# Performance work log

Hardware: AMD Instinct MI355X
Metric: run time of the kernel (lower is better)

## Reference

```python
import jax, jax.numpy as jnp
import numpy as np

PIXEL_SIZE = 0.1
PI = 3.141592653589793


def setup_inputs() -> dict:
    key = jax.random.key(0)
    batch = jax.random.normal(key, (128, 1, 512, 512), dtype=jnp.float32)
    return {"batch": batch}


def _hann_window(roi):
    # lin = linspace(-roi/2, roi/2, roi); r[i,j] = sqrt(lin[j]^2 + lin[i]^2)
    lin = jnp.linspace(-roi / 2, roi / 2, roi, dtype=jnp.float32)
    r = jnp.sqrt(lin[None, :] ** 2 + lin[:, None] ** 2)
    hann = 0.5 * (1.0 + jnp.cos(PI * r / (roi / 2)))
    hann = jnp.where(r > roi / 2, 0.0, hann)
    return hann  # [roi, roi]


def _radial_segments(roi, n_freq):
    # radialDst = round(sqrt(xx^2 + yy^2)) with x = arange(-cx, roi-cx)
    cx = roi // 2
    x = np.arange(-cx, roi - cx, dtype=np.float64)
    xx, yy = np.meshgrid(x, x, indexing="ij")
    rad = np.round(np.sqrt(xx ** 2 + yy ** 2)).astype(np.int32)
    # bins >= n_freq go into an overflow segment that is discarded
    seg = np.where(rad < n_freq, rad, n_freq)
    return jnp.asarray(seg.ravel())


def reference(batch):
    px = PIXEL_SIZE
    roi = batch.shape[-1]
    cx = roi // 2
    n_freq = cx + 1
    nyquist = 1.0 / (2.0 * px)

    # subtract per-ROI mean
    batch_nm = batch - jnp.mean(batch, axis=(2, 3), keepdims=True)

    # Hann-windowed 2D power spectrum, averaged over realizations
    hann = _hann_window(roi)[None, None, :, :]
    F = jnp.fft.fftshift(jnp.fft.fft2(batch_nm * hann, axes=(2, 3)), axes=(2, 3))
    ps = jnp.mean(jnp.abs(F) ** 2, axis=0)            # [1, roi, roi]
    nps2D = (px ** 2 / roi ** 2) * jnp.squeeze(ps)    # [roi, roi]

    # single-pass radial mean binning (replaces per-k boolean-mask loop)
    seg = _radial_segments(roi, n_freq)
    flat = nps2D.ravel()
    sums = jax.ops.segment_sum(flat, seg, num_segments=n_freq + 1)[:n_freq]
    counts = jax.ops.segment_sum(jnp.ones_like(flat), seg, num_segments=n_freq + 1)[:n_freq]
    nps1D = sums / counts

    f1D = jnp.linspace(0.0, nyquist, n_freq, dtype=jnp.float32)
    return nps1D, nps2D, f1D
```

## Files before the change

kernel.cpp:

```cpp
#include <hip/hip_runtime.h>
#include <hip/hip_fp16.h>

#define N 512
#define NF 257
#define NB 128
#define PI_F 3.14159265358979323846f
#define C_SQ2 0.70710678118654752440f

__device__ __forceinline__ float2 cmul(float2 a, float2 b) {
    return make_float2(a.x * b.x - a.y * b.y, a.x * b.y + a.y * b.x);
}
__device__ __forceinline__ void bf(float2& a, float2& b) {
    float2 t = b;
    b = make_float2(a.x - t.x, a.y - t.y);
    a = make_float2(a.x + t.x, a.y + t.y);
}
__device__ __forceinline__ void bf_tw(float2& a, float2& b, float2 w) {
    float2 t = cmul(b, w);
    b = make_float2(a.x - t.x, a.y - t.y);
    a = make_float2(a.x + t.x, a.y + t.y);
}
__device__ __forceinline__ void bf_ni(float2& a, float2& b) {
    float2 t = make_float2(b.y, -b.x);
    b = make_float2(a.x - t.x, a.y - t.y);
    a = make_float2(a.x + t.x, a.y + t.y);
}
__device__ __forceinline__ void lds_order() {
    asm volatile("" ::: "memory");
}

__device__ __forceinline__ void fft_phaseA(float2 v[8]) {
    const float2 w64  = make_float2(C_SQ2, -C_SQ2);
    const float2 w192 = make_float2(-C_SQ2, -C_SQ2);
    bf(v[0], v[1]); bf(v[2], v[3]); bf(v[4], v[5]); bf(v[6], v[7]);
    bf(v[0], v[2]); bf_ni(v[1], v[3]); bf(v[4], v[6]); bf_ni(v[5], v[7]);
    bf(v[0], v[4]); bf_tw(v[1], v[5], w64); bf_ni(v[2], v[6]); bf_tw(v[3], v[7], w192);
}
__device__ __forceinline__ void fft_phaseBC(float2 v[8], float2 W1, float2 W1a,
                                            float2 W1n, float2 W1c, float2 W2,
                                            float2 W2n, float2 W3) {
    bf_tw(v[0], v[1], W3); bf_tw(v[2], v[3], W3); bf_tw(v[4], v[5], W3); bf_tw(v[6], v[7], W3);
    bf_tw(v[0], v[2], W2); bf_tw(v[1], v[3], W2n); bf_tw(v[4], v[6], W2); bf_tw(v[5], v[7], W2n);
    bf_tw(v[0], v[4], W1); bf_tw(v[1], v[5], W1a); bf_tw(v[2], v[6], W1n); bf_tw(v[3], v[7], W1c);
}

__device__ __forceinline__ void fft512_core(float2 v[8], float2* st, int l) {
    const float2 w64  = make_float2(C_SQ2, -C_SQ2);
    const float2 w192 = make_float2(-C_SQ2, -C_SQ2);
    int g = l >> 3, r = l & 7;
    lds_order();
    fft_phaseA(v);
#pragma unroll
    for (int e = 0; e < 8; e++) st[9 * l + e] = v[e];
    lds_order();
#pragma unroll
    for (int t = 0; t < 8; t++) v[t] = st[72 * g + 9 * t + r];
    float sn, cs;
    __sincosf(-(PI_F / 32.0f) * (float)r, &sn, &cs);
    float2 W1 = make_float2(cs, sn);
    float2 W2 = cmul(W1, W1);
    float2 W3 = cmul(W2, W2);
    float2 W2n = make_float2(W2.y, -W2.x);
    float2 W1a = cmul(W1, w64);
    float2 W1n = make_float2(W1.y, -W1.x);
    float2 W1c = cmul(W1, w192);
    fft_phaseBC(v, W1, W1a, W1n, W1c, W2, W2n, W3);
    lds_order();
#pragma unroll
    for (int t = 0; t < 8; t++) st[72 * g + 9 * t + r] = v[t];
    lds_order();
#pragma unroll
    for (int t = 0; t < 8; t++) v[t] = st[72 * t + l + (l >> 3)];
    __sincosf(-(PI_F / 256.0f) * (float)l, &sn, &cs);
    float2 Wc = make_float2(cs, sn);
    float2 w2 = cmul(Wc, Wc);
    float2 w4 = cmul(w2, w2);
    float2 w2n = make_float2(w2.y, -w2.x);
    float2 Wca = cmul(Wc, w64);
    float2 Wcn = make_float2(Wc.y, -Wc.x);
    float2 Wcc = cmul(Wc, w192);
    fft_phaseBC(v, Wc, Wca, Wcn, Wcc, w2, w2n, w4);
}

__device__ __forceinline__ void fft512_x2(float2 va[8], float2 vb[8], float2* st, int l) {
    const float2 w64  = make_float2(C_SQ2, -C_SQ2);
    const float2 w192 = make_float2(-C_SQ2, -C_SQ2);
    int g = l >> 3, r = l & 7;
    fft_phaseA(va); fft_phaseA(vb);
    lds_order();
#pragma unroll
    for (int e = 0; e < 8; e++) st[9 * l + e] = va[e];
    lds_order();
#pragma unroll
    for (int t = 0; t < 8; t++) va[t] = st[72 * g + 9 * t + r];
    lds_order();
#pragma unroll
    for (int e = 0; e < 8; e++) st[9 * l + e] = vb[e];
    lds_order();
#pragma unroll
    for (int t = 0; t < 8; t++) vb[t] = st[72 * g + 9 * t + r];
    float sn, cs;
    __sincosf(-(PI_F / 32.0f) * (float)r, &sn, &cs);
    float2 W1 = make_float2(cs, sn);
    float2 W2 = cmul(W1, W1);
    float2 W3 = cmul(W2, W2);
    float2 W2n = make_float2(W2.y, -W2.x);
    float2 W1a = cmul(W1, w64);
    float2 W1n = make_float2(W1.y, -W1.x);
    float2 W1c = cmul(W1, w192);
    fft_phaseBC(va, W1, W1a, W1n, W1c, W2, W2n, W3);
    fft_phaseBC(vb, W1, W1a, W1n, W1c, W2, W2n, W3);
    lds_order();
#pragma unroll
    for (int t = 0; t < 8; t++) st[72 * g + 9 * t + r] = va[t];
    lds_order();
#pragma unroll
    for (int t = 0; t < 8; t++) va[t] = st[72 * t + l + (l >> 3)];
    lds_order();
#pragma unroll
    for (int t = 0; t < 8; t++) st[72 * g + 9 * t + r] = vb[t];
    lds_order();
#pragma unroll
    for (int t = 0; t < 8; t++) vb[t] = st[72 * t + l + (l >> 3)];
    __sincosf(-(PI_F / 256.0f) * (float)l, &sn, &cs);
    float2 Wc = make_float2(cs, sn);
    float2 w2 = cmul(Wc, Wc);
    float2 w4 = cmul(w2, w2);
    float2 w2n = make_float2(w2.y, -w2.x);
    float2 Wca = cmul(Wc, w64);
    float2 Wcn = make_float2(Wc.y, -Wc.x);
    float2 Wcc = cmul(Wc, w192);
    fft_phaseBC(va, Wc, Wca, Wcn, Wcc, w2, w2n, w4);
    fft_phaseBC(vb, Wc, Wca, Wcn, Wcc, w2, w2n, w4);
}

__device__ __forceinline__ void unpack_rows(const float2 v[8], __half2* tile,
                                            int lr0, int lr1, int l, int sl) {
#pragma unroll
    for (int t = 0; t <= 4; t++) {
        float2 a = v[7 - t];
        float zfx = __shfl(a.x, sl);
        float zfy = __shfl(a.y, sl);
        if (l == 0) { float2 o = v[(8 - t) & 7]; zfx = o.x; zfy = o.y; }
        float2 z = v[t];
        int col = 64 * t + l;
        if (col < NF) {
            tile[lr0 * 265 + col] = __floats2half2_rn(0.5f * (z.x + zfx), 0.5f * (z.y - zfy));
            tile[lr1 * 265 + col] = __floats2half2_rn(0.5f * (z.y + zfy), 0.5f * (zfx - z.x));
        }
    }
}

__global__ void zero_kernel(float* __restrict__ accH, float* __restrict__ bins,
                            float* __restrict__ meanacc) {
    int i = blockIdx.x * blockDim.x + threadIdx.x;
    if (i < NF * N) accH[i] = 0.0f;
    if (i < 2 * (NF + 1)) bins[i] = 0.0f;
    if (i < NB) meanacc[i] = 0.0f;
}

__global__ __launch_bounds__(256) void hanntab_kernel(float* __restrict__ htab) {
    int i = blockIdx.x * 256 + threadIdx.x;
    int r = i >> 9, c = i & (N - 1);
    const float step = (float)N / (float)(N - 1);
    float a = -0.5f * (float)N + (float)r * step;
    float b = -0.5f * (float)N + (float)c * step;
    float rr = sqrtf(a * a + b * b);
    float h = (rr > 256.0f) ? 0.0f : 0.5f * (1.0f + cosf(rr * (PI_F / 256.0f)));
    htab[i] = h;
}

__global__ __launch_bounds__(512) void hannfft_kernel(const float* __restrict__ htab,
                                                      float2* __restrict__ Hrow) {
    __shared__ float sm[9216];
    int tid = threadIdx.x;
    int w = tid >> 6, l = tid & 63;
    int rowbase = blockIdx.x << 4;
    int r1 = rowbase + 2 * w;
    int rl = __brev((unsigned)l) >> 26;
    const int bre[8] = {0, 4, 2, 6, 1, 5, 3, 7};
    const float* h1 = htab + (size_t)r1 * N + rl;
    const float* h2 = h1 + N;

    float2 v[8];
#pragma unroll
    for (int e = 0; e < 8; e++) {
        int o = bre[e] << 6;
        v[e] = make_float2(h1[o], h2[o]);
    }

    float2* st = (float2*)sm + w * 576;
    fft512_core(v, st, l);
    __syncthreads();

    float* tre = sm;
    float* tim = sm + 4240;
    int lr0 = 2 * w, lr1 = lr0 + 1;
    int sl = (64 - l) & 63;
#pragma unroll
    for (int t = 0; t <= 4; t++) {
        float2 a = v[7 - t];
        float zfx = __shfl(a.x, sl);
        float zfy = __shfl(a.y, sl);
        if (l == 0) { float2 o = v[(8 - t) & 7]; zfx = o.x; zfy = o.y; }
        float2 z = v[t];
        int col = 64 * t + l;
        if (col < NF) {
            tre[lr0 * 265 + col] = 0.5f * (z.x + zfx);
            tim[lr0 * 265 + col] = 0.5f * (z.y - zfy);
            tre[lr1 * 265 + col] = 0.5f * (z.y + zfy);
            tim[lr1 * 265 + col] = 0.5f * (zfx - z.x);
        }
    }
    __syncthreads();

    int c0 = tid >> 4, rr = tid & 15;
#pragma unroll
    for (int it = 0; it < 9; it++) {
        int c = it * 32 + c0;
        if (c < NF) {
            float2 val = make_float2(tre[rr * 265 + c], tim[rr * 265 + c]);
            Hrow[(size_t)c * N + rowbase + rr] = val;
        }
    }
}

__global__ __launch_bounds__(512, 4) void rowfft_kernel(const float* __restrict__ x,
                                                        const float* __restrict__ htab,
                                                        float* __restrict__ meanacc,
                                                        __half2* __restrict__ inter) {
    __shared__ float sm[9216];
    __shared__ float redsum[8];
    int tid = threadIdx.x;
    int w = tid >> 6, l = tid & 63;
    int img = blockIdx.x >> 4;
    int rowbase = (blockIdx.x & 15) << 5;
    int r1 = rowbase + 4 * w;
    int rl = __brev((unsigned)l) >> 26;
    const int bre[8] = {0, 4, 2, 6, 1, 5, 3, 7};
    const float* xp = x + ((size_t)img * N + r1) * N + rl;
    const float* hp = htab + (size_t)r1 * N + rl;

    float ax[4][8], hx[4][8];
#pragma unroll
    for (int j = 0; j < 4; j++)
#pragma unroll
        for (int e = 0; e < 8; e++) ax[j][e] = xp[j * N + (bre[e] << 6)];
#pragma unroll
    for (int j = 0; j < 4; j++)
#pragma unroll
        for (int e = 0; e < 8; e++) hx[j][e] = hp[j * N + (bre[e] << 6)];
    __builtin_amdgcn_sched_barrier(0);

    float rsum = 0.0f;
#pragma unroll
    for (int j = 0; j < 4; j++)
#pragma unroll
        for (int e = 0; e < 8; e++) rsum += ax[j][e];

    float2 va[8], vb[8];
#pragma unroll
    for (int e = 0; e < 8; e++) {
        va[e] = make_float2(ax[0][e] * hx[0][e], ax[1][e] * hx[1][e]);
        vb[e] = make_float2(ax[2][e] * hx[2][e], ax[3][e] * hx[3][e]);
    }

#pragma unroll
    for (int off = 32; off > 0; off >>= 1) rsum += __shfl_down(rsum, off);
    if (l == 0) redsum[w] = rsum;

    float2* st = (float2*)sm + w * 576;
    fft512_x2(va, vb, st, l);
    __syncthreads();
    if (tid == 0) {
        float s = 0.0f;
#pragma unroll
        for (int i = 0; i < 8; i++) s += redsum[i];
        atomicAdd(meanacc + img, s);
    }

    __half2* tile = (__half2*)sm;
    int sl = (64 - l) & 63;
    unpack_rows(va, tile, 4 * w, 4 * w + 1, l, sl);
    unpack_rows(vb, tile, 4 * w + 2, 4 * w + 3, l, sl);
    __syncthreads();

    int c0 = tid >> 5, rr = tid & 31;
#pragma unroll
    for (int it = 0; it < 17; it++) {
        int c = it * 16 + c0;
        if (c < NF) {
            inter[((size_t)img * NF + c) * N + rowbase + rr] = tile[rr * 265 + c];
        }
    }
}

__global__ __launch_bounds__(256, 4) void colfft_kernel(const __half2* __restrict__ inter,
                                                        const float2* __restrict__ Hrow,
                                                        const float* __restrict__ meanacc,
                                                        float* __restrict__ accH) {
    __shared__ float sm[4608];
    int tid = threadIdx.x;
    int w = tid >> 6, l = tid & 63;
    int col = blockIdx.x * 4 + w;
    int colc = col < NF ? col : NF - 1;
    int b0 = blockIdx.y * 4;
    float2* st = (float2*)sm + w * 576;
    int rl = __brev((unsigned)l) >> 26;
    const int bre[8] = {0, 4, 2, 6, 1, 5, 3, 7};

    float2 hc[8];
    const float2* hp = Hrow + (size_t)colc * N + rl;
#pragma unroll
    for (int e = 0; e < 8; e++) hc[e] = hp[bre[e] << 6];

    float mn[4];
#pragma unroll
    for (int i = 0; i < 4; i++)
        mn[i] = meanacc[b0 + i] * (1.0f / ((float)N * (float)N));

    float pw[8];
#pragma unroll
    for (int t = 0; t < 8; t++) pw[t] = 0.0f;

    const size_t istr = (size_t)NF * N;
    const __half2* base = inter + ((size_t)b0 * NF + colc) * N + rl;

    __half2 cA[8], cB[8], nA[8], nB[8];
#pragma unroll
    for (int e = 0; e < 8; e++) {
        cA[e] = base[bre[e] << 6];
        cB[e] = base[istr + (bre[e] << 6)];
    }
    __builtin_amdgcn_sched_barrier(0);

#pragma unroll
    for (int it = 0; it < 2; it++) {
        if (it == 0) {
#pragma unroll
            for (int e = 0; e < 8; e++) {
                nA[e] = base[2 * istr + (bre[e] << 6)];
                nB[e] = base[3 * istr + (bre[e] << 6)];
            }
        }
        float mA = mn[2 * it], mB = mn[2 * it + 1];
        float2 va[8], vb[8];
#pragma unroll
        for (int e = 0; e < 8; e++) {
            float2 zA = __half22float2(cA[e]);
            float2 zB = __half22float2(cB[e]);
            va[e] = make_float2(zA.x - mA * hc[e].x, zA.y - mA * hc[e].y);
            vb[e] = make_float2(zB.x - mB * hc[e].x, zB.y - mB * hc[e].y);
        }
        fft512_x2(va, vb, st, l);
#pragma unroll
        for (int t = 0; t < 8; t++)
            pw[t] += va[t].x * va[t].x + va[t].y * va[t].y
                   + vb[t].x * vb[t].x + vb[t].y * vb[t].y;
#pragma unroll
        for (int e = 0; e < 8; e++) { cA[e] = nA[e]; cB[e] = nB[e]; }
    }

    if (col < NF) {
#pragma unroll
        for (int t = 0; t < 8; t++)
            atomicAdd(&accH[(size_t)col * N + 64 * t + l], pw[t]);
    }
}

__global__ __launch_bounds__(256) void finalize2d_kernel(const float* __restrict__ accH,
                                                         float* __restrict__ out2d,
                                                         float* __restrict__ bins) {
    __shared__ float lsum[NF];
    __shared__ float lcnt[NF];
    int t = threadIdx.x;
    for (int i = t; i < NF; i += 256) { lsum[i] = 0.0f; lcnt[i] = 0.0f; }
    __syncthreads();
    const float scale = (0.1f * 0.1f) / ((float)N * (float)N) / (float)NB;
    int idx = blockIdx.x * 256 + t;
    int stride = gridDim.x * 256;
    for (int p = idx; p < N * N; p += stride) {
        int i = p >> 9, j = p & (N - 1);
        int jm = (j + 256) & 511;
        int col, k;
        if (jm < NF) { col = jm; k = (i + 256) & 511; }
        else         { col = 256 - j; k = (256 - i) & 511; }
        float v = accH[((size_t)col << 9) + k] * scale;
        out2d[p] = v;
        float xi = (float)(i - 256), yj = (float)(j - 256);
        int rad = (int)rintf(sqrtf(xi * xi + yj * yj));
        if (rad < NF) { atomicAdd(&lsum[rad], v); atomicAdd(&lcnt[rad], 1.0f); }
    }
    __syncthreads();
    for (int i = t; i < NF; i += 256) {
        if (lsum[i] != 0.0f || lcnt[i] != 0.0f) {
            atomicAdd(&bins[i], lsum[i]);
            atomicAdd(&bins[NF + 1 + i], lcnt[i]);
        }
    }
}

__global__ void finalize1d_kernel(const float* __restrict__ bins, float* __restrict__ out) {
    int t = blockIdx.x * blockDim.x + threadIdx.x;
    if (t < NF) {
        out[t] = bins[t] / bins[NF + 1 + t];
        out[NF + N * N + t] = (float)t * (5.0f / 256.0f);
    }
}

extern "C" void kernel_launch(void* const* d_in, const int* in_sizes, int n_in,
                              void* d_out, int out_size, void* d_ws, size_t ws_size,
                              hipStream_t stream) {
    const float* x = (const float*)d_in[0];
    float* out = (float*)d_out;
    char* ws = (char*)d_ws;

    float* accH    = (float*)ws;
    float* meanacc = (float*)(ws + (size_t)NF * N * sizeof(float));
    float* bins    = meanacc + NB;
    size_t off_h = (size_t)NF * N * sizeof(float) + NB * sizeof(float)
                   + 2 * (NF + 1) * sizeof(float);
    off_h = (off_h + 255) & ~(size_t)255;
    float2* Hrow = (float2*)(ws + off_h);
    size_t off_t = off_h + (size_t)NF * N * sizeof(float2);
    off_t = (off_t + 255) & ~(size_t)255;
    float* htab = (float*)(ws + off_t);
    size_t off_inter = off_t + (size_t)N * N * sizeof(float);
    off_inter = (off_inter + 255) & ~(size_t)255;
    __half2* inter = (__half2*)(ws + off_inter);

    zero_kernel<<<dim3((NF * N + 255) / 256), dim3(256), 0, stream>>>(accH, bins, meanacc);
    hanntab_kernel<<<dim3(N * N / 256), dim3(256), 0, stream>>>(htab);
    hannfft_kernel<<<dim3(32), dim3(512), 0, stream>>>(htab, Hrow);
    rowfft_kernel<<<dim3(NB * 16), dim3(512), 0, stream>>>(x, htab, meanacc, inter);
    colfft_kernel<<<dim3(65, 32), dim3(256), 0, stream>>>(inter, Hrow, meanacc, accH);
    finalize2d_kernel<<<dim3(256), dim3(256), 0, stream>>>(accH, out + NF, bins);
    finalize1d_kernel<<<dim3(2), dim3(256), 0, stream>>>(bins, out);
}
```

Before: 256.1 us.

## Use packed float2 vector type, fuse zero into hann table kernel, retune launches

Replaces the float2 struct with an ext_vector_type float2 so complex arithmetic can lower to packed FP32 instructions (v_pk_fma/v_pk_add). Merges the zeroing kernel into the Hann table kernel to remove one launch. Raises rowfft occupancy hint from 4 to 6 waves per SIMD and doubles finalize2d grid size. The occupancy hint may force register spills, and the finalize2d grid change depends on kernel internals not shown.

```diff
diff --git a/kernel.cpp b/kernel.cpp
--- a/kernel.cpp
+++ b/kernel.cpp
@@ -7,46 +7,49 @@
 #define PI_F 3.14159265358979323846f
 #define C_SQ2 0.70710678118654752440f
 
-__device__ __forceinline__ float2 cmul(float2 a, float2 b) {
-    return make_float2(a.x * b.x - a.y * b.y, a.x * b.y + a.y * b.x);
-}
-__device__ __forceinline__ void bf(float2& a, float2& b) {
-    float2 t = b;
-    b = make_float2(a.x - t.x, a.y - t.y);
-    a = make_float2(a.x + t.x, a.y + t.y);
-}
-__device__ __forceinline__ void bf_tw(float2& a, float2& b, float2 w) {
-    float2 t = cmul(b, w);
-    b = make_float2(a.x - t.x, a.y - t.y);
-    a = make_float2(a.x + t.x, a.y + t.y);
-}
-__device__ __forceinline__ void bf_ni(float2& a, float2& b) {
-    float2 t = make_float2(b.y, -b.x);
-    b = make_float2(a.x - t.x, a.y - t.y);
-    a = make_float2(a.x + t.x, a.y + t.y);
+typedef float f2 __attribute__((ext_vector_type(2)));
+__device__ __forceinline__ f2 F2(float x, float y) { f2 r; r.x = x; r.y = y; return r; }
+
+__device__ __forceinline__ f2 cmul(f2 a, f2 b) {
+    return a.xx * b + F2(-a.y, a.y) * b.yx;
+}
+__device__ __forceinline__ void bf(f2& a, f2& b) {
+    f2 t = b;
+    b = a - t;
+    a = a + t;
+}
+__device__ __forceinline__ void bf_tw(f2& a, f2& b, f2 w) {
+    f2 t = cmul(b, w);
+    b = a - t;
+    a = a + t;
+}
+__device__ __forceinline__ void bf_ni(f2& a, f2& b) {
+    f2 t = F2(b.y, -b.x);
+    b = a - t;
+    a = a + t;
 }
 __device__ __forceinline__ void lds_order() {
     asm volatile("" ::: "memory");
 }
 
-__device__ __forceinline__ void fft_phaseA(float2 v[8]) {
-    const float2 w64  = make_float2(C_SQ2, -C_SQ2);
-    const float2 w192 = make_float2(-C_SQ2, -C_SQ2);
+__device__ __forceinline__ void fft_phaseA(f2 v[8]) {
+    const f2 w64  = F2(C_SQ2, -C_SQ2);
+    const f2 w192 = F2(-C_SQ2, -C_SQ2);
     bf(v[0], v[1]); bf(v[2], v[3]); bf(v[4], v[5]); bf(v[6], v[7]);
     bf(v[0], v[2]); bf_ni(v[1], v[3]); bf(v[4], v[6]); bf_ni(v[5], v[7]);
     bf(v[0], v[4]); bf_tw(v[1], v[5], w64); bf_ni(v[2], v[6]); bf_tw(v[3], v[7], w192);
 }
-__device__ __forceinline__ void fft_phaseBC(float2 v[8], float2 W1, float2 W1a,
-                                            float2 W1n, float2 W1c, float2 W2,
-                                            float2 W2n, float2 W3) {
+__device__ __forceinline__ void fft_phaseBC(f2 v[8], f2 W1, f2 W1a,
+                                            f2 W1n, f2 W1c, f2 W2,
+                                            f2 W2n, f2 W3) {
     bf_tw(v[0], v[1], W3); bf_tw(v[2], v[3], W3); bf_tw(v[4], v[5], W3); bf_tw(v[6], v[7], W3);
     bf_tw(v[0], v[2], W2); bf_tw(v[1], v[3], W2n); bf_tw(v[4], v[6], W2); bf_tw(v[5], v[7], W2n);
     bf_tw(v[0], v[4], W1); bf_tw(v[1], v[5], W1a); bf_tw(v[2], v[6], W1n); bf_tw(v[3], v[7], W1c);
 }
 
-__device__ __forceinline__ void fft512_core(float2 v[8], float2* st, int l) {
-    const float2 w64  = make_float2(C_SQ2, -C_SQ2);
-    const float2 w192 = make_float2(-C_SQ2, -C_SQ2);
+__device__ __forceinline__ void fft512_core(f2 v[8], f2* st, int l) {
+    const f2 w64  = F2(C_SQ2, -C_SQ2);
+    const f2 w192 = F2(-C_SQ2, -C_SQ2);
     int g = l >> 3, r = l & 7;
     lds_order();
     fft_phaseA(v);
@@ -57,13 +60,13 @@
     for (int t = 0; t < 8; t++) v[t] = st[72 * g + 9 * t + r];
     float sn, cs;
     __sincosf(-(PI_F / 32.0f) * (float)r, &sn, &cs);
-    float2 W1 = make_float2(cs, sn);
-    float2 W2 = cmul(W1, W1);
-    float2 W3 = cmul(W2, W2);
-    float2 W2n = make_float2(W2.y, -W2.x);
-    float2 W1a = cmul(W1, w64);
-    float2 W1n = make_float2(W1.y, -W1.x);
-    float2 W1c = cmul(W1, w192);
+    f2 W1 = F2(cs, sn);
+    f2 W2 = cmul(W1, W1);
+    f2 W3 = cmul(W2, W2);
+    f2 W2n = F2(W2.y, -W2.x);
+    f2 W1a = cmul(W1, w64);
+    f2 W1n = F2(W1.y, -W1.x);
+    f2 W1c = cmul(W1, w192);
     fft_phaseBC(v, W1, W1a, W1n, W1c, W2, W2n, W3);
     lds_order();
 #pragma unroll
@@ -72,19 +75,19 @@
 #pragma unroll
     for (int t = 0; t < 8; t++) v[t] = st[72 * t + l + (l >> 3)];
     __sincosf(-(PI_F / 256.0f) * (float)l, &sn, &cs);
-    float2 Wc = make_float2(cs, sn);
-    float2 w2 = cmul(Wc, Wc);
-    float2 w4 = cmul(w2, w2);
-    float2 w2n = make_float2(w2.y, -w2.x);
-    float2 Wca = cmul(Wc, w64);
-    float2 Wcn = make_float2(Wc.y, -Wc.x);
-    float2 Wcc = cmul(Wc, w192);
+    f2 Wc = F2(cs, sn);
+    f2 w2 = cmul(Wc, Wc);
+    f2 w4 = cmul(w2, w2);
+    f2 w2n = F2(w2.y, -w2.x);
+    f2 Wca = cmul(Wc, w64);
+    f2 Wcn = F2(Wc.y, -Wc.x);
+    f2 Wcc = cmul(Wc, w192);
     fft_phaseBC(v, Wc, Wca, Wcn, Wcc, w2, w2n, w4);
 }
 
-__device__ __forceinline__ void fft512_x2(float2 va[8], float2 vb[8], float2* st, int l) {
-    const float2 w64  = make_float2(C_SQ2, -C_SQ2);
-    const float2 w192 = make_float2(-C_SQ2, -C_SQ2);
+__device__ __forceinline__ void fft512_x2(f2 va[8], f2 vb[8], f2* st, int l) {
+    const f2 w64  = F2(C_SQ2, -C_SQ2);
+    const f2 w192 = F2(-C_SQ2, -C_SQ2);
     int g = l >> 3, r = l & 7;
     fft_phaseA(va); fft_phaseA(vb);
     lds_order();
@@ -101,13 +104,13 @@
     for (int t = 0; t < 8; t++) vb[t] = st[72 * g + 9 * t + r];
     float sn, cs;
     __sincosf(-(PI_F / 32.0f) * (float)r, &sn, &cs);
-    float2 W1 = make_float2(cs, sn);
-    float2 W2 = cmul(W1, W1);
-    float2 W3 = cmul(W2, W2);
-    float2 W2n = make_float2(W2.y, -W2.x);
-    float2 W1a = cmul(W1, w64);
-    float2 W1n = make_float2(W1.y, -W1.x);
-    float2 W1c = cmul(W1, w192);
+    f2 W1 = F2(cs, sn);
+    f2 W2 = cmul(W1, W1);
+    f2 W3 = cmul(W2, W2);
+    f2 W2n = F2(W2.y, -W2.x);
+    f2 W1a = cmul(W1, w64);
+    f2 W1n = F2(W1.y, -W1.x);
+    f2 W1c = cmul(W1, w192);
     fft_phaseBC(va, W1, W1a, W1n, W1c, W2, W2n, W3);
     fft_phaseBC(vb, W1, W1a, W1n, W1c, W2, W2n, W3);
     lds_order();
@@ -123,26 +126,26 @@
 #pragma unroll
     for (int t = 0; t < 8; t++) vb[t] = st[72 * t + l + (l >> 3)];
     __sincosf(-(PI_F / 256.0f) * (float)l, &sn, &cs);
-    float2 Wc = make_float2(cs, sn);
-    float2 w2 = cmul(Wc, Wc);
-    float2 w4 = cmul(w2, w2);
-    float2 w2n = make_float2(w2.y, -w2.x);
-    float2 Wca = cmul(Wc, w64);
-    float2 Wcn = make_float2(Wc.y, -Wc.x);
-    float2 Wcc = cmul(Wc, w192);
+    f2 Wc = F2(cs, sn);
+    f2 w2 = cmul(Wc, Wc);
+    f2 w4 = cmul(w2, w2);
+    f2 w2n = F2(w2.y, -w2.x);
+    f2 Wca = cmul(Wc, w64);
+    f2 Wcn = F2(Wc.y, -Wc.x);
+    f2 Wcc = cmul(Wc, w192);
     fft_phaseBC(va, Wc, Wca, Wcn, Wcc, w2, w2n, w4);
     fft_phaseBC(vb, Wc, Wca, Wcn, Wcc, w2, w2n, w4);
 }
 
-__device__ __forceinline__ void unpack_rows(const float2 v[8], __half2* tile,
+__device__ __forceinline__ void unpack_rows(const f2 v[8], __half2* tile,
                                             int lr0, int lr1, int l, int sl) {
 #pragma unroll
     for (int t = 0; t <= 4; t++) {
-        float2 a = v[7 - t];
+        f2 a = v[7 - t];
         float zfx = __shfl(a.x, sl);
         float zfy = __shfl(a.y, sl);
-        if (l == 0) { float2 o = v[(8 - t) & 7]; zfx = o.x; zfy = o.y; }
-        float2 z = v[t];
+        if (l == 0) { f2 o = v[(8 - t) & 7]; zfx = o.x; zfy = o.y; }
+        f2 z = v[t];
         int col = 64 * t + l;
         if (col < NF) {
             tile[lr0 * 265 + col] = __floats2half2_rn(0.5f * (z.x + zfx), 0.5f * (z.y - zfy));
@@ -151,15 +154,10 @@
     }
 }
 
-__global__ void zero_kernel(float* __restrict__ accH, float* __restrict__ bins,
-                            float* __restrict__ meanacc) {
-    int i = blockIdx.x * blockDim.x + threadIdx.x;
-    if (i < NF * N) accH[i] = 0.0f;
-    if (i < 2 * (NF + 1)) bins[i] = 0.0f;
-    if (i < NB) meanacc[i] = 0.0f;
-}
-
-__global__ __launch_bounds__(256) void hanntab_kernel(float* __restrict__ htab) {
+__global__ __launch_bounds__(256) void hanntab_zero_kernel(float* __restrict__ htab,
+                                                           float* __restrict__ accH,
+                                                           float* __restrict__ bins,
+                                                           float* __restrict__ meanacc) {
     int i = blockIdx.x * 256 + threadIdx.x;
     int r = i >> 9, c = i & (N - 1);
     const float step = (float)N / (float)(N - 1);
@@ -168,11 +166,14 @@
     float rr = sqrtf(a * a + b * b);
     float h = (rr > 256.0f) ? 0.0f : 0.5f * (1.0f + cosf(rr * (PI_F / 256.0f)));
     htab[i] = h;
+    if (i < NF * N) accH[i] = 0.0f;
+    if (i < 2 * (NF + 1)) bins[i] = 0.0f;
+    if (i < NB) meanacc[i] = 0.0f;
 }
 
 __global__ __launch_bounds__(512) void hannfft_kernel(const float* __restrict__ htab,
-                                                      float2* __restrict__ Hrow) {
-    __shared__ float sm[9216];
+                                                      f2* __restrict__ Hrow) {
+    __shared__ __align__(16) float sm[9216];
     int tid = threadIdx.x;
     int w = tid >> 6, l = tid & 63;
     int rowbase = blockIdx.x << 4;
@@ -182,14 +183,14 @@
     const float* h1 = htab + (size_t)r1 * N + rl;
     const float* h2 = h1 + N;
 
-    float2 v[8];
+    f2 v[8];
 #pragma unroll
     for (int e = 0; e < 8; e++) {
         int o = bre[e] << 6;
-        v[e] = make_float2(h1[o], h2[o]);
-    }
-
-    float2* st = (float2*)sm + w * 576;
+        v[e] = F2(h1[o], h2[o]);
+    }
+
+    f2* st = (f2*)sm + w * 576;
     fft512_core(v, st, l);
     __syncthreads();
 
@@ -199,11 +200,11 @@
     int sl = (64 - l) & 63;
 #pragma unroll
     for (int t = 0; t <= 4; t++) {
-        float2 a = v[7 - t];
+        f2 a = v[7 - t];
         float zfx = __shfl(a.x, sl);
         float zfy = __shfl(a.y, sl);
-        if (l == 0) { float2 o = v[(8 - t) & 7]; zfx = o.x; zfy = o.y; }
-        float2 z = v[t];
+        if (l == 0) { f2 o = v[(8 - t) & 7]; zfx = o.x; zfy = o.y; }
+        f2 z = v[t];
         int col = 64 * t + l;
         if (col < NF) {
             tre[lr0 * 265 + col] = 0.5f * (z.x + zfx);
@@ -219,17 +220,16 @@
     for (int it = 0; it < 9; it++) {
         int c = it * 32 + c0;
         if (c < NF) {
-            float2 val = make_float2(tre[rr * 265 + c], tim[rr * 265 + c]);
-            Hrow[(size_t)c * N + rowbase + rr] = val;
-        }
-    }
-}
-
-__global__ __launch_bounds__(512, 4) void rowfft_kernel(const float* __restrict__ x,
+            Hrow[(size_t)c * N + rowbase + rr] = F2(tre[rr * 265 + c], tim[rr * 265 + c]);
+        }
+    }
+}
+
+__global__ __launch_bounds__(512, 6) void rowfft_kernel(const float* __restrict__ x,
                                                         const float* __restrict__ htab,
                                                         float* __restrict__ meanacc,
                                                         __half2* __restrict__ inter) {
-    __shared__ float sm[9216];
+    __shared__ __align__(16) float sm[9216];
     __shared__ float redsum[8];
     int tid = threadIdx.x;
     int w = tid >> 6, l = tid & 63;
@@ -258,18 +258,18 @@
 #pragma unroll
         for (int e = 0; e < 8; e++) rsum += ax[j][e];
 
-    float2 va[8], vb[8];
+    f2 va[8], vb[8];
 #pragma unroll
     for (int e = 0; e < 8; e++) {
-        va[e] = make_float2(ax[0][e] * hx[0][e], ax[1][e] * hx[1][e]);
-        vb[e] = make_float2(ax[2][e] * hx[2][e], ax[3][e] * hx[3][e]);
+        va[e] = F2(ax[0][e] * hx[0][e], ax[1][e] * hx[1][e]);
+        vb[e] = F2(ax[2][e] * hx[2][e], ax[3][e] * hx[3][e]);
     }
 
 #pragma unroll
     for (int off = 32; off > 0; off >>= 1) rsum += __shfl_down(rsum, off);
     if (l == 0) redsum[w] = rsum;
 
-    float2* st = (float2*)sm + w * 576;
+    f2* st = (f2*)sm + w * 576;
     fft512_x2(va, vb, st, l);
     __syncthreads();
     if (tid == 0) {
@@ -296,21 +296,21 @@
 }
 
 __global__ __launch_bounds__(256, 4) void colfft_kernel(const __half2* __restrict__ inter,
-                                                        const float2* __restrict__ Hrow,
+                                                        const f2* __restrict__ Hrow,
                                                         const float* __restrict__ meanacc,
                                                         float* __restrict__ accH) {
-    __shared__ float sm[4608];
+    __shared__ __align__(16) float sm[4608];
     int tid = threadIdx.x;
     int w = tid >> 6, l = tid & 63;
     int col = blockIdx.x * 4 + w;
     int colc = col < NF ? col : NF - 1;
     int b0 = blockIdx.y * 4;
-    float2* st = (float2*)sm + w * 576;
+    f2* st = (f2*)sm + w * 576;
     int rl = __brev((unsigned)l) >> 26;
     const int bre[8] = {0, 4, 2, 6, 1, 5, 3, 7};
 
-    float2 hc[8];
-    const float2* hp = Hrow + (size_t)colc * N + rl;
+    f2 hc[8];
+    const f2* hp = Hrow + (size_t)colc * N + rl;
 #pragma unroll
     for (int e = 0; e < 8; e++) hc[e] = hp[bre[e] << 6];
 
@@ -344,13 +344,13 @@
             }
         }
         float mA = mn[2 * it], mB = mn[2 * it + 1];
-        float2 va[8], vb[8];
+        f2 va[8], vb[8];
 #pragma unroll
         for (int e = 0; e < 8; e++) {
             float2 zA = __half22float2(cA[e]);
             float2 zB = __half22float2(cB[e]);
-            va[e] = make_float2(zA.x - mA * hc[e].x, zA.y - mA * hc[e].y);
-            vb[e] = make_float2(zB.x - mB * hc[e].x, zB.y - mB * hc[e].y);
+            va[e] = F2(zA.x, zA.y) - mA * hc[e];
+            vb[e] = F2(zB.x, zB.y) - mB * hc[e];
         }
         fft512_x2(va, vb, st, l);
 #pragma unroll
@@ -421,19 +421,18 @@
     size_t off_h = (size_t)NF * N * sizeof(float) + NB * sizeof(float)
                    + 2 * (NF + 1) * sizeof(float);
     off_h = (off_h + 255) & ~(size_t)255;
-    float2* Hrow = (float2*)(ws + off_h);
-    size_t off_t = off_h + (size_t)NF * N * sizeof(float2);
+    f2* Hrow = (f2*)(ws + off_h);
+    size_t off_t = off_h + (size_t)NF * N * sizeof(f2);
     off_t = (off_t + 255) & ~(size_t)255;
     float* htab = (float*)(ws + off_t);
     size_t off_inter = off_t + (size_t)N * N * sizeof(float);
     off_inter = (off_inter + 255) & ~(size_t)255;
     __half2* inter = (__half2*)(ws + off_inter);
 
-    zero_kernel<<<dim3((NF * N + 255) / 256), dim3(256), 0, stream>>>(accH, bins, meanacc);
-    hanntab_kernel<<<dim3(N * N / 256), dim3(256), 0, stream>>>(htab);
+    hanntab_zero_kernel<<<dim3(N * N / 256), dim3(256), 0, stream>>>(htab, accH, bins, meanacc);
     hannfft_kernel<<<dim3(32), dim3(512), 0, stream>>>(htab, Hrow);
     rowfft_kernel<<<dim3(NB * 16), dim3(512), 0, stream>>>(x, htab, meanacc, inter);
     colfft_kernel<<<dim3(65, 32), dim3(256), 0, stream>>>(inter, Hrow, meanacc, accH);
-    finalize2d_kernel<<<dim3(256), dim3(256), 0, stream>>>(accH, out + NF, bins);
+    finalize2d_kernel<<<dim3(512), dim3(256), 0, stream>>>(accH, out + NF, bins);
     finalize1d_kernel<<<dim3(2), dim3(256), 0, stream>>>(bins, out);
 }
```

Measured after the change: 264.1 us. 1.03x slower.
